# Kernel tuning notes

Hardware: AMD Instinct MI355X
Metric: run time of the kernel (lower is better)

The kernel has to match this reference:

```python
import jax, jax.numpy as jnp
import numpy as np

DIM = 1024
HEADS = 16
HEAD_DIM = DIM // HEADS

def setup_inputs() -> dict:
    key = jax.random.key(0)
    ks = jax.random.split(key, 5)
    x = jax.random.normal(ks[0], (4, 2048, DIM), dtype=jnp.float32)
    s = DIM ** -0.5
    W_qkv = jax.random.normal(ks[1], (DIM, 3 * DIM), dtype=jnp.float32) * s
    b_qkv = jnp.zeros((3 * DIM,), dtype=jnp.float32)
    W_proj = jax.random.normal(ks[2], (DIM, DIM), dtype=jnp.float32) * s
    b_proj = jnp.zeros((DIM,), dtype=jnp.float32)
    return {"x": x, "W_qkv": W_qkv, "b_qkv": b_qkv, "W_proj": W_proj, "b_proj": b_proj}

def reference(x, W_qkv, b_qkv, W_proj, b_proj):
    B, S, D = x.shape
    scale = HEAD_DIM ** -0.5
    qkv = x @ W_qkv + b_qkv                      # [B,S,3D]
    q, k, v = jnp.split(qkv, 3, axis=-1)         # each [B,S,D]
    def heads(t):
        return t.reshape(B, S, HEADS, HEAD_DIM).transpose(0, 2, 1, 3)  # [B,H,S,d]
    q, k, v = heads(q), heads(k), heads(v)
    attn = jnp.einsum('bhqd,bhkd->bhqk', q, k) * scale
    attn = jax.nn.softmax(attn, axis=-1)
    out = jnp.einsum('bhqk,bhkd->bhqd', attn, v)  # [B,H,S,d]
    out = out.transpose(0, 2, 1, 3).reshape(B, S, D)
    return out @ W_proj + b_proj
```

## Files before the change

kernel.cpp:

```cpp
#include <hip/hip_runtime.h>
#include <hip/hip_bf16.h>
#include <cstdint>


#define SEQ   2048
#define NDIM  1024
#define HEADS 16
#define HD    64

typedef __attribute__((ext_vector_type(8))) short bf16x8;
typedef __attribute__((ext_vector_type(4))) float f32x4;

typedef __attribute__((address_space(1))) void glob_void;
typedef __attribute__((address_space(3))) void lds_void;

__device__ __forceinline__ short f2b(float f) {
    uint32_t u = __float_as_uint(f);
    u += 0x7FFF + ((u >> 16) & 1);
    return (short)(u >> 16);
}
__device__ __forceinline__ uint32_t cvtpk(float lo, float hi) {
    uint32_t d;
    asm("v_cvt_pk_bf16_f32 %0, %1, %2" : "=v"(d) : "v"(lo), "v"(hi));
    return d;
}

__global__ __launch_bounds__(256) void sentinel_k(float* __restrict__ out, float v, int n) {
    const int i = blockIdx.x * 256 + threadIdx.x;
    if (i < n) out[i] = v;
}

__global__ __launch_bounds__(256) void transpose_k(const float* __restrict__ W,
                                                   short* __restrict__ WT,
                                                   int R, int C) {
    __shared__ short t[32][33];
    const int bx = blockIdx.x * 32;
    const int by = blockIdx.y * 32;
    const int tx = threadIdx.x, ty = threadIdx.y;
#pragma unroll
    for (int i = 0; i < 32; i += 8)
        t[ty + i][tx] = f2b(W[(size_t)(by + ty + i) * C + bx + tx]);
    __syncthreads();
#pragma unroll
    for (int i = 0; i < 32; i += 8)
        WT[(size_t)(bx + ty + i) * R + by + tx] = t[tx][ty + i];
}

__global__ __launch_bounds__(256) void gemm_bt(const void* __restrict__ A,
                                               const short* __restrict__ BT,
                                               const float* __restrict__ bias,
                                               void* __restrict__ Cout,
                                               int N, int K, int lda,
                                               int amode, int cmode) {
    __shared__ short As[128 * 64];
    __shared__ short Bs[128 * 64];

    const short* Ab = (const short*)A;
    const float* Af = (const float*)A;

    const int tid  = threadIdx.x;
    const int lane = tid & 63;
    const int wid  = tid >> 6;
    const int ln16 = lane & 15;
    const int quad = lane >> 4;
    const int wm = (wid & 1) * 64;
    const int wn = (wid >> 1) * 64;
    const int bm = blockIdx.y * 128;
    const int bn = blockIdx.x * 128;

    f32x4 acc[4][4];
#pragma unroll
    for (int i = 0; i < 4; ++i)
#pragma unroll
        for (int j = 0; j < 4; ++j) {
            acc[i][j][0] = 0.f; acc[i][j][1] = 0.f; acc[i][j][2] = 0.f; acc[i][j][3] = 0.f;
        }

    const int rbase = tid >> 3;
    const int k8    = (tid & 7) * 8;

    for (int ks = 0; ks < K; ks += 64) {
        __syncthreads();
#pragma unroll
        for (int i = 0; i < 4; ++i) {
            const int row = i * 32 + rbase;
            const int c   = i * 256 + tid;
            const short* gb = BT + (size_t)(bn + row) * K + ks + k8;
            __builtin_amdgcn_global_load_lds((glob_void*)gb, (lds_void*)(Bs + c * 8), 16, 0, 0);
        }
        if (amode) {
#pragma unroll
            for (int i = 0; i < 4; ++i) {
                const int row = i * 32 + rbase;
                const int c   = i * 256 + tid;
                const short* ga = Ab + (size_t)(bm + row) * lda + ks + k8;
                __builtin_amdgcn_global_load_lds((glob_void*)ga, (lds_void*)(As + c * 8), 16, 0, 0);
            }
        } else {
#pragma unroll
            for (int i = 0; i < 4; ++i) {
                const int row = i * 32 + rbase;
                const int c   = i * 256 + tid;
                const float* ga = Af + (size_t)(bm + row) * lda + ks + k8;
                const float4 f0 = *(const float4*)ga;
                const float4 f1 = *(const float4*)(ga + 4);
                union { bf16x8 v; short s[8]; } u;
                u.s[0] = f2b(f0.x); u.s[1] = f2b(f0.y); u.s[2] = f2b(f0.z); u.s[3] = f2b(f0.w);
                u.s[4] = f2b(f1.x); u.s[5] = f2b(f1.y); u.s[6] = f2b(f1.z); u.s[7] = f2b(f1.w);
                *(bf16x8*)(As + c * 8) = u.v;
            }
        }
        __syncthreads();

#pragma unroll
        for (int kk = 0; kk < 2; ++kk) {
            bf16x8 a[4], b[4];
#pragma unroll
            for (int t = 0; t < 4; ++t) {
                a[t] = *(const bf16x8*)(As + (wm + t * 16 + ln16) * 64 + kk * 32 + quad * 8);
                b[t] = *(const bf16x8*)(Bs + (wn + t * 16 + ln16) * 64 + kk * 32 + quad * 8);
            }
#pragma unroll
            for (int tm = 0; tm < 4; ++tm)
#pragma unroll
                for (int tn = 0; tn < 4; ++tn)
                    acc[tm][tn] = __builtin_amdgcn_mfma_f32_16x16x32_bf16(a[tm], b[tn], acc[tm][tn], 0, 0, 0);
        }
    }

#pragma unroll
    for (int tm = 0; tm < 4; ++tm) {
        const int row = bm + wm + tm * 16 + quad * 4;
#pragma unroll
        for (int tn = 0; tn < 4; ++tn) {
            const int col = bn + wn + tn * 16 + ln16;
            const float bv = bias[col];
#pragma unroll
            for (int r = 0; r < 4; ++r) {
                const float cv = acc[tm][tn][r] + bv;
                const size_t idx = (size_t)(row + r) * N + col;
                if (cmode) ((float*)Cout)[idx] = cv;
                else       ((short*)Cout)[idx] = f2b(cv);
            }
        }
    }
}

__global__ __launch_bounds__(256, 3) void attn_k(short* qkv) {
    __shared__ __attribute__((aligned(16))) char smem[32768];
    uint32_t* VTw  = (uint32_t*)smem;
    uint32_t* Psw  = (uint32_t*)(smem + 16384);
    float*    Obuf = (float*)smem;
    float*    lred = (float*)(smem + 17408);

    const int tid  = threadIdx.x;
    const int lane = tid & 63;
    const int wid  = tid >> 6;
    const int ln16 = lane & 15;
    const int quad = lane >> 4;
    const int sw   = ln16 & 7;

    const int bx = blockIdx.x;
    const int qt = bx & 31;
    const int bh = bx >> 5;
    const int b  = bh >> 4;
    const int h  = bh & 15;
    const int q0 = qt * 64;

    const size_t row0 = ((size_t)b * SEQ) * 3072 + h * HD;
    const int slab = wid * 32;

    bf16x8 qf[4][2];
#pragma unroll
    for (int qg = 0; qg < 4; ++qg) {
        const short* qr = qkv + row0 + (size_t)(q0 + qg * 16 + ln16) * 3072 + quad * 8;
        qf[qg][0] = *(const bf16x8*)(qr);
        qf[qg][1] = *(const bf16x8*)(qr + 32);
    }

    float l[4] = {0.f, 0.f, 0.f, 0.f};
    f32x4 o[4][4];
#pragma unroll
    for (int t = 0; t < 4; ++t)
#pragma unroll
        for (int qg = 0; qg < 4; ++qg) {
            o[t][qg][0] = 0.f; o[t][qg][1] = 0.f; o[t][qg][2] = 0.f; o[t][qg][3] = 0.f;
        }

    const int vpair = wid * 16 + ln16;
    const int vd16  = quad * 16;
    const short* kbase = qkv + row0 + (size_t)(slab + ln16) * 3072 + 1024 + quad * 8;
    const short* vbase = qkv + row0 + 2048 + vd16;

    const float C1 = 0.18033688f;
    const float C0 = -17.3123405f;

    union U4 { uint4 u; uint32_t w[4]; };
    U4 va0, va1, vb0, vb1;
    {
        const short* gv = vbase + (size_t)(2 * vpair) * 3072;
        va0.u = *(const uint4*)gv;
        va1.u = *(const uint4*)(gv + 8);
        vb0.u = *(const uint4*)(gv + 3072);
        vb1.u = *(const uint4*)(gv + 3072 + 8);
    }

    for (int kb = 0; kb < SEQ; kb += 128) {
        const short* kr = kbase + (size_t)kb * 3072;
        const bf16x8 kf0 = *(const bf16x8*)(kr);
        const bf16x8 kf1 = *(const bf16x8*)(kr + 32);
        const bf16x8 kf2 = *(const bf16x8*)(kr + 16 * 3072);
        const bf16x8 kf3 = *(const bf16x8*)(kr + 16 * 3072 + 32);

#pragma unroll
        for (int j = 0; j < 8; ++j) {
            const uint32_t sel = (j & 1) ? 0x07060302u : 0x05040100u;
            const int wsw = vpair ^ (j << 2) ^ (quad << 4);
            VTw[(vd16 + j) * 64 + wsw]     = __builtin_amdgcn_perm(vb0.w[j >> 1], va0.w[j >> 1], sel);
            VTw[(vd16 + 8 + j) * 64 + wsw] = __builtin_amdgcn_perm(vb1.w[j >> 1], va1.w[j >> 1], sel);
        }

#pragma unroll
        for (int kg = 0; kg < 2; ++kg) {
            const bf16x8 a0 = kg ? kf2 : kf0;
            const bf16x8 a1 = kg ? kf3 : kf1;
#pragma unroll
            for (int qg = 0; qg < 4; ++qg) {
                f32x4 z; z[0] = 0.f; z[1] = 0.f; z[2] = 0.f; z[3] = 0.f;
                z = __builtin_amdgcn_mfma_f32_16x16x32_bf16(a0, qf[qg][0], z, 0, 0, 0);
                z = __builtin_amdgcn_mfma_f32_16x16x32_bf16(a1, qf[qg][1], z, 0, 0, 0);
                const float p0 = __builtin_amdgcn_exp2f(fmaf(z[0], C1, C0));
                const float p1 = __builtin_amdgcn_exp2f(fmaf(z[1], C1, C0));
                const float p2 = __builtin_amdgcn_exp2f(fmaf(z[2], C1, C0));
                const float p3 = __builtin_amdgcn_exp2f(fmaf(z[3], C1, C0));
                l[qg] += (p0 + p1) + (p2 + p3);
                const int prow = qg * 16 + ln16;
                const int wb   = wid * 16 + kg * 8 + quad * 2;
                uint2 pv;
                pv.x = cvtpk(p0, p1);
                pv.y = cvtpk(p2, p3);
                *(uint2*)(Psw + prow * 64 + (wb ^ (sw << 2))) = pv;
            }
        }

        {
            const int kb2 = (kb + 128) & (SEQ - 1);
            const short* gv = vbase + (size_t)(kb2 + 2 * vpair) * 3072;
            va0.u = *(const uint4*)gv;
            va1.u = *(const uint4*)(gv + 8);
            vb0.u = *(const uint4*)(gv + 3072);
            vb1.u = *(const uint4*)(gv + 3072 + 8);
        }

        bf16x8 bp[4];
#pragma unroll
        for (int qg = 0; qg < 4; ++qg)
            bp[qg] = *(const bf16x8*)(Psw + (qg * 16 + ln16) * 64 + ((wid * 16 + quad * 4) ^ (sw << 2)));
        __builtin_amdgcn_s_setprio(1);
#pragma unroll
        for (int t = 0; t < 4; ++t) {
            const bf16x8 av = *(const bf16x8*)(VTw + (t * 16 + ln16) * 64
                                               + ((wid * 16 + quad * 4) ^ (sw << 2) ^ (t << 4)));
#pragma unroll
            for (int qg = 0; qg < 4; ++qg)
                o[t][qg] = __builtin_amdgcn_mfma_f32_16x16x32_bf16(av, bp[qg], o[t][qg], 0, 0, 0);
        }
        __builtin_amdgcn_s_setprio(0);
    }

    __syncthreads();
#pragma unroll
    for (int qg = 0; qg < 4; ++qg) {
        l[qg] += __shfl_xor(l[qg], 16, 64);
        l[qg] += __shfl_xor(l[qg], 32, 64);
    }
    if (quad == 0) {
#pragma unroll
        for (int qg = 0; qg < 4; ++qg)
            lred[wid * 64 + qg * 16 + ln16] = l[qg];
    }
    for (int w = 0; w < 4; ++w) {
        if (wid == w) {
#pragma unroll
            for (int t = 0; t < 4; ++t)
#pragma unroll
                for (int qg = 0; qg < 4; ++qg) {
                    float* dst = &Obuf[(qg * 16 + ln16) * 68 + t * 16 + quad * 4];
                    if (w == 0) {
                        *(f32x4*)dst = o[t][qg];
                    } else {
                        f32x4 prev = *(const f32x4*)dst;
                        prev[0] += o[t][qg][0]; prev[1] += o[t][qg][1];
                        prev[2] += o[t][qg][2]; prev[3] += o[t][qg][3];
                        *(f32x4*)dst = prev;
                    }
                }
        }
        __syncthreads();
    }

    const int q  = tid & 63;
    const int dc = (tid >> 6) * 16;
    const float linv = 1.0f / (lred[q] + lred[64 + q] + lred[128 + q] + lred[192 + q]);
    const float* ob = Obuf + q * 68 + dc;
    const f32x4 o0 = *(const f32x4*)ob;
    const f32x4 o1 = *(const f32x4*)(ob + 4);
    const f32x4 o2 = *(const f32x4*)(ob + 8);
    const f32x4 o3 = *(const f32x4*)(ob + 12);
    union { uint4 u[2]; uint32_t w[8]; } outp;
    outp.w[0] = cvtpk(o0[0] * linv, o0[1] * linv);
    outp.w[1] = cvtpk(o0[2] * linv, o0[3] * linv);
    outp.w[2] = cvtpk(o1[0] * linv, o1[1] * linv);
    outp.w[3] = cvtpk(o1[2] * linv, o1[3] * linv);
    outp.w[4] = cvtpk(o2[0] * linv, o2[1] * linv);
    outp.w[5] = cvtpk(o2[2] * linv, o2[3] * linv);
    outp.w[6] = cvtpk(o3[0] * linv, o3[1] * linv);
    outp.w[7] = cvtpk(o3[2] * linv, o3[3] * linv);
    uint4* dst = (uint4*)(qkv + row0 + (size_t)(q0 + q) * 3072 + dc);
    dst[0] = outp.u[0];
    dst[1] = outp.u[1];
}

extern "C" void kernel_launch(void* const* d_in, const int* in_sizes, int n_in,
                              void* d_out, int out_size, void* d_ws, size_t ws_size,
                              hipStream_t stream) {
    const float* x     = (const float*)d_in[0];
    const float* Wqkv  = (const float*)d_in[1];
    const float* bqkv  = (const float*)d_in[2];
    const float* Wproj = (const float*)d_in[3];
    const float* bproj = (const float*)d_in[4];
    float* out = (float*)d_out;

    int bad = -1;
    if (n_in != 5) bad = 9;
    else {
        const int want[5] = {8388608, 3145728, 3072, 1048576, 1024};
        for (int i = 0; i < 5; ++i) if (in_sizes[i] != want[i]) { bad = i; break; }
        if (bad < 0 && out_size != 8388608) bad = 8;
    }
    if (bad >= 0) {
        sentinel_k<<<(out_size + 255) / 256, 256, 0, stream>>>(out, 1000.0f + 100.0f * bad, out_size);
        return;
    }

    char* ws = (char*)d_ws;
    short* wqkvT  = (short*)(ws);
    short* wprojT = (short*)(ws + 6291456);
    short* qkv    = (short*)(ws + 8388608);

    transpose_k<<<dim3(96, 32), dim3(32, 8), 0, stream>>>(Wqkv, wqkvT, 1024, 3072);
    transpose_k<<<dim3(32, 32), dim3(32, 8), 0, stream>>>(Wproj, wprojT, 1024, 1024);

    gemm_bt<<<dim3(3072 / 128, 8192 / 128), 256, 0, stream>>>(
        x, wqkvT, bqkv, qkv, 3072, 1024, 1024, 0, 0);

    attn_k<<<dim3(4 * HEADS * (SEQ / 64)), 256, 0, stream>>>(qkv);

    gemm_bt<<<dim3(1024 / 128, 8192 / 128), 256, 0, stream>>>(
        qkv, wprojT, bproj, out, 1024, 1024, 3072, 1, 1);
}
```

Measured before the change: 345.5 us.

## Pre-convert x to bf16, XCD-aware block remap, and prefetch K in attention

New measurement: 363.1 us. 5.1% more time.

```diff
diff --git a/kernel.cpp b/kernel.cpp
--- a/kernel.cpp
+++ b/kernel.cpp
@@ -28,6 +28,18 @@
 __global__ __launch_bounds__(256) void sentinel_k(float* __restrict__ out, float v, int n) {
     const int i = blockIdx.x * 256 + threadIdx.x;
     if (i < n) out[i] = v;
+}
+
+__global__ __launch_bounds__(256) void convert_k(const float* __restrict__ in,
+                                                 short* __restrict__ out, int n8) {
+    const int i = blockIdx.x * 256 + threadIdx.x;
+    if (i >= n8) return;
+    const float4 f0 = *(const float4*)(in + (size_t)i * 8);
+    const float4 f1 = *(const float4*)(in + (size_t)i * 8 + 4);
+    union { bf16x8 v; short s[8]; } u;
+    u.s[0] = f2b(f0.x); u.s[1] = f2b(f0.y); u.s[2] = f2b(f0.z); u.s[3] = f2b(f0.w);
+    u.s[4] = f2b(f1.x); u.s[5] = f2b(f1.y); u.s[6] = f2b(f1.z); u.s[7] = f2b(f1.w);
+    *(bf16x8*)(out + (size_t)i * 8) = u.v;
 }
 
 __global__ __launch_bounds__(256) void transpose_k(const float* __restrict__ W,
@@ -65,8 +77,14 @@
     const int quad = lane >> 4;
     const int wm = (wid & 1) * 64;
     const int wn = (wid >> 1) * 64;
-    const int bm = blockIdx.y * 128;
-    const int bn = blockIdx.x * 128;
+
+    const int nbx = gridDim.x;
+    const int nwg = gridDim.x * gridDim.y;
+    int lin = blockIdx.y * nbx + blockIdx.x;
+    if ((nwg & 7) == 0)
+        lin = (lin & 7) * (nwg >> 3) + (lin >> 3);
+    const int bm = (lin / nbx) * 128;
+    const int bn = (lin % nbx) * 128;
 
     f32x4 acc[4][4];
 #pragma unroll
@@ -160,12 +178,13 @@
     const int quad = lane >> 4;
     const int sw   = ln16 & 7;
 
-    const int bx = blockIdx.x;
-    const int qt = bx & 31;
-    const int bh = bx >> 5;
-    const int b  = bh >> 4;
-    const int h  = bh & 15;
-    const int q0 = qt * 64;
+    const int i0  = blockIdx.x;
+    const int xcd = i0 & 7;
+    const int qt  = (i0 >> 3) & 31;
+    const int bh  = (i0 >> 8) * 8 + xcd;
+    const int b   = bh >> 4;
+    const int h   = bh & 15;
+    const int q0  = qt * 64;
 
     const size_t row0 = ((size_t)b * SEQ) * 3072 + h * HD;
     const int slab = wid * 32;
@@ -197,7 +216,13 @@
 
     union U4 { uint4 u; uint32_t w[4]; };
     U4 va0, va1, vb0, vb1;
+    bf16x8 kf0, kf1, kf2, kf3;
     {
+        const short* kr = kbase;
+        kf0 = *(const bf16x8*)(kr);
+        kf1 = *(const bf16x8*)(kr + 32);
+        kf2 = *(const bf16x8*)(kr + 16 * 3072);
+        kf3 = *(const bf16x8*)(kr + 16 * 3072 + 32);
         const short* gv = vbase + (size_t)(2 * vpair) * 3072;
         va0.u = *(const uint4*)gv;
         va1.u = *(const uint4*)(gv + 8);
@@ -206,20 +231,6 @@
     }
 
     for (int kb = 0; kb < SEQ; kb += 128) {
-        const short* kr = kbase + (size_t)kb * 3072;
-        const bf16x8 kf0 = *(const bf16x8*)(kr);
-        const bf16x8 kf1 = *(const bf16x8*)(kr + 32);
-        const bf16x8 kf2 = *(const bf16x8*)(kr + 16 * 3072);
-        const bf16x8 kf3 = *(const bf16x8*)(kr + 16 * 3072 + 32);
-
-#pragma unroll
-        for (int j = 0; j < 8; ++j) {
-            const uint32_t sel = (j & 1) ? 0x07060302u : 0x05040100u;
-            const int wsw = vpair ^ (j << 2) ^ (quad << 4);
-            VTw[(vd16 + j) * 64 + wsw]     = __builtin_amdgcn_perm(vb0.w[j >> 1], va0.w[j >> 1], sel);
-            VTw[(vd16 + 8 + j) * 64 + wsw] = __builtin_amdgcn_perm(vb1.w[j >> 1], va1.w[j >> 1], sel);
-        }
-
 #pragma unroll
         for (int kg = 0; kg < 2; ++kg) {
             const bf16x8 a0 = kg ? kf2 : kf0;
@@ -244,6 +255,22 @@
         }
 
         {
+            const short* kr = kbase + (size_t)((kb + 128) & (SEQ - 1)) * 3072;
+            kf0 = *(const bf16x8*)(kr);
+            kf1 = *(const bf16x8*)(kr + 32);
+            kf2 = *(const bf16x8*)(kr + 16 * 3072);
+            kf3 = *(const bf16x8*)(kr + 16 * 3072 + 32);
+        }
+
+#pragma unroll
+        for (int j = 0; j < 8; ++j) {
+            const uint32_t sel = (j & 1) ? 0x07060302u : 0x05040100u;
+            const int wsw = vpair ^ (j << 2) ^ (quad << 4);
+            VTw[(vd16 + j) * 64 + wsw]     = __builtin_amdgcn_perm(vb0.w[j >> 1], va0.w[j >> 1], sel);
+            VTw[(vd16 + 8 + j) * 64 + wsw] = __builtin_amdgcn_perm(vb1.w[j >> 1], va1.w[j >> 1], sel);
+        }
+
+        {
             const int kb2 = (kb + 128) & (SEQ - 1);
             const short* gv = vbase + (size_t)(kb2 + 2 * vpair) * 3072;
             va0.u = *(const uint4*)gv;
@@ -256,6 +283,7 @@
 #pragma unroll
         for (int qg = 0; qg < 4; ++qg)
             bp[qg] = *(const bf16x8*)(Psw + (qg * 16 + ln16) * 64 + ((wid * 16 + quad * 4) ^ (sw << 2)));
+
         __builtin_amdgcn_s_setprio(1);
 #pragma unroll
         for (int t = 0; t < 4; ++t) {
@@ -347,12 +375,20 @@
     short* wqkvT  = (short*)(ws);
     short* wprojT = (short*)(ws + 6291456);
     short* qkv    = (short*)(ws + 8388608);
+    short* xb     = (short*)(ws + 58720256);
+    const bool have_xb = (ws_size >= 58720256ull + 16777216ull);
 
     transpose_k<<<dim3(96, 32), dim3(32, 8), 0, stream>>>(Wqkv, wqkvT, 1024, 3072);
     transpose_k<<<dim3(32, 32), dim3(32, 8), 0, stream>>>(Wproj, wprojT, 1024, 1024);
 
-    gemm_bt<<<dim3(3072 / 128, 8192 / 128), 256, 0, stream>>>(
-        x, wqkvT, bqkv, qkv, 3072, 1024, 1024, 0, 0);
+    if (have_xb) {
+        convert_k<<<4096, 256, 0, stream>>>(x, xb, 1048576);
+        gemm_bt<<<dim3(3072 / 128, 8192 / 128), 256, 0, stream>>>(
+            xb, wqkvT, bqkv, qkv, 3072, 1024, 1024, 1, 0);
+    } else {
+        gemm_bt<<<dim3(3072 / 128, 8192 / 128), 256, 0, stream>>>(
+            x, wqkvT, bqkv, qkv, 3072, 1024, 1024, 0, 0);
+    }
 
     attn_k<<<dim3(4 * HEADS * (SEQ / 64)), 256, 0, stream>>>(qkv);
 
```
